# Kernel optimization log

Measured on AMD Instinct MI355X. Metric: run time of the kernel, lower is better.

## Reference

```python
import jax, jax.numpy as jnp
import numpy as np

N_NODES = 100000
N_FEATURES = 64
HIDDEN = 32
N_CLASSES = 10


def cheb_conv(x, row, col, W0, W1, b):
    """PyG ChebConv with K=2, sym normalization, lambda_max=2.0.

    L = I - D^-1/2 A D^-1/2 ; L_hat = 2L/lambda_max - I = -D^-1/2 A D^-1/2.
    out = x @ W0 + (L_hat x) @ W1 + b
    """
    N = x.shape[0]
    ew = jnp.where(row == col, 0.0, 1.0)  # remove_self_loops
    deg = jax.ops.segment_sum(ew, row, num_segments=N)
    dis = jnp.where(deg > 0, jax.lax.rsqrt(jnp.maximum(deg, 1.0)), 0.0)
    w = -(dis[row] * ew * dis[col])  # [E] scaled-Laplacian off-diagonal weights
    Tx1 = jax.ops.segment_sum(w[:, None] * x[row], col, num_segments=N)  # [N, F]
    return x @ W0 + Tx1 @ W1 + b


def _glorot(key, shape):
    fan_in, fan_out = shape
    s = jnp.sqrt(6.0 / (fan_in + fan_out))
    return jax.random.uniform(key, shape, jnp.float32, -s, s)


def setup_inputs() -> dict:
    key = jax.random.key(0)
    ks = jax.random.split(key, 8)
    x = jax.random.normal(ks[0], (N_NODES, N_FEATURES), dtype=jnp.float32)
    edge_index = jax.random.randint(ks[1], (2, 3200000), 0, N_NODES, dtype=jnp.int64)
    return {
        "x": x,
        "edge_index": edge_index,
        "W0_1": _glorot(ks[2], (N_FEATURES, HIDDEN)),
        "W1_1": _glorot(ks[3], (N_FEATURES, HIDDEN)),
        "b1": jnp.zeros((HIDDEN,), jnp.float32),
        "W0_2": _glorot(ks[4], (HIDDEN, N_CLASSES)),
        "W1_2": _glorot(ks[5], (HIDDEN, N_CLASSES)),
        "b2": jnp.zeros((N_CLASSES,), jnp.float32),
    }


def reference(x, edge_index, W0_1, W1_1, b1, W0_2, W1_2, b2):
    row, col = edge_index[0], edge_index[1]
    h = jax.nn.relu(cheb_conv(x, row, col, W0_1, W1_1, b1))
    x_latent = h
    # dropout is identity in eval mode
    out = cheb_conv(h, row, col, W0_2, W1_2, b2)
    return jax.nn.log_softmax(out, axis=1), x_latent
```

## Files before the change

kernel.cpp:

```cpp
#include <hip/hip_runtime.h>

#define NN   100000
#define FIN  64
#define HID  32
#define NCLS 10
#define BW   256
#define NB   391
#define HB   512

__global__ __launch_bounds__(256) void hist2_kernel(
        const int* __restrict__ row, const int* __restrict__ col,
        int* __restrict__ ghc, int* __restrict__ ghr, int E, int chunk) {
    __shared__ int lhc[NB], lhr[NB];
    for (int t = threadIdx.x; t < NB; t += 256) { lhc[t] = 0; lhr[t] = 0; }
    __syncthreads();
    int k = blockIdx.x;
    int base = k * chunk;
    int lim = base + chunk; if (lim > E) lim = E;
    for (int e = base + threadIdx.x; e < lim; e += 256) {
        int r = row[e], c = col[e];
        if (r != c) {
            atomicAdd(&lhc[c >> 8], 1);
            atomicAdd(&lhr[r >> 8], 1);
        }
    }
    __syncthreads();
    for (int t = threadIdx.x; t < NB; t += 256) {
        ghc[t * HB + k] = lhc[t];
        ghr[t * HB + k] = lhr[t];
    }
}

__global__ __launch_bounds__(512) void coffs_kernel(
        int* __restrict__ ghc, int* __restrict__ ghr,
        int* __restrict__ ctot, int* __restrict__ rtot) {
    __shared__ int sh[HB];
    int b = blockIdx.x, t = threadIdx.x;
    int v = ghc[b * HB + t];
    sh[t] = v;
    __syncthreads();
    for (int off = 1; off < HB; off <<= 1) {
        int u = (t >= off) ? sh[t - off] : 0;
        __syncthreads(); sh[t] += u; __syncthreads();
    }
    ghc[b * HB + t] = sh[t] - v;
    if (t == HB - 1) ctot[b] = sh[t];
    __syncthreads();
    int w = ghr[b * HB + t];
    sh[t] = w;
    __syncthreads();
    for (int off = 1; off < HB; off <<= 1) {
        int u = (t >= off) ? sh[t - off] : 0;
        __syncthreads(); sh[t] += u; __syncthreads();
    }
    ghr[b * HB + t] = sh[t] - w;
    if (t == HB - 1) rtot[b] = sh[t];
}

__global__ __launch_bounds__(512) void bscan_kernel(
        const int* __restrict__ ctot, const int* __restrict__ rtot,
        int* __restrict__ cbptr, int* __restrict__ rbptr,
        int* __restrict__ colptr) {
    __shared__ int sh[512];
    int t = threadIdx.x;
    int v = (t < NB) ? ctot[t] : 0;
    sh[t] = v;
    __syncthreads();
    for (int off = 1; off < 512; off <<= 1) {
        int u = (t >= off) ? sh[t - off] : 0;
        __syncthreads(); sh[t] += u; __syncthreads();
    }
    if (t < NB) cbptr[t] = sh[t] - v;
    if (t == NB - 1) { cbptr[NB] = sh[t]; colptr[NN] = sh[t]; }
    __syncthreads();
    int w = (t < NB) ? rtot[t] : 0;
    sh[t] = w;
    __syncthreads();
    for (int off = 1; off < 512; off <<= 1) {
        int u = (t >= off) ? sh[t - off] : 0;
        __syncthreads(); sh[t] += u; __syncthreads();
    }
    if (t < NB) rbptr[t] = sh[t] - w;
    if (t == NB - 1) rbptr[NB] = sh[t];
}

__global__ __launch_bounds__(256) void bucket2_kernel(
        const int* __restrict__ row, const int* __restrict__ col,
        const int* __restrict__ ghc, const int* __restrict__ ghr,
        const int* __restrict__ cbptr, const int* __restrict__ rbptr,
        int* __restrict__ pk, unsigned char* __restrict__ rkb,
        int E, int chunk) {
    __shared__ int lcc[NB], lcr[NB];
    int k = blockIdx.x;
    for (int t = threadIdx.x; t < NB; t += 256) {
        lcc[t] = cbptr[t] + ghc[t * HB + k];
        lcr[t] = rbptr[t] + ghr[t * HB + k];
    }
    __syncthreads();
    int base = k * chunk;
    int lim = base + chunk; if (lim > E) lim = E;
    for (int e = base + threadIdx.x; e < lim; e += 256) {
        int r = row[e], c = col[e];
        if (r != c) {
            int pc = atomicAdd(&lcc[c >> 8], 1);
            pk[pc] = (r << 8) | (c & 255);
            int pr = atomicAdd(&lcr[r >> 8], 1);
            rkb[pr] = (unsigned char)(r & 255);
        }
    }
}

__global__ __launch_bounds__(256) void countR_kernel(
        const unsigned char* __restrict__ rkb, const int* __restrict__ rbptr,
        float* __restrict__ dis) {
    __shared__ int cnt[BW];
    int b = blockIdx.x, t = threadIdx.x;
    cnt[t] = 0;
    __syncthreads();
    int s = rbptr[b], e = rbptr[b + 1];
    for (int i = s + t; i < e; i += 256) atomicAdd(&cnt[rkb[i]], 1);
    __syncthreads();
    int d = (b << 8) + t;
    if (d < NN) {
        int c = cnt[t];
        dis[d] = c > 0 ? rsqrtf((float)c) : 0.f;
    }
}

__global__ __launch_bounds__(256) void place2_kernel(
        const int* __restrict__ pk, const int* __restrict__ cbptr,
        int* __restrict__ colptr, int* __restrict__ srow) {
    __shared__ int lh[BW];
    __shared__ int incl[BW];
    __shared__ int lcur[BW];
    int b = blockIdx.x, t = threadIdx.x;
    int start = cbptr[b], end = cbptr[b + 1];
    lh[t] = 0;
    __syncthreads();
    for (int i = start + t; i < end; i += 256)
        atomicAdd(&lh[pk[i] & 255], 1);
    __syncthreads();
    int own = lh[t];
    incl[t] = own;
    __syncthreads();
    for (int off = 1; off < 256; off <<= 1) {
        int v = (t >= off) ? incl[t - off] : 0;
        __syncthreads(); incl[t] += v; __syncthreads();
    }
    int excl = start + incl[t] - own;
    int d = (b << 8) + t;
    if (d < NN) colptr[d] = excl;
    lcur[t] = excl;
    __syncthreads();
    for (int i = start + t; i < end; i += 256) {
        int p = pk[i];
        int pos = atomicAdd(&lcur[p & 255], 1);
        srow[pos] = p >> 8;
    }
}

__global__ __launch_bounds__(256) void mm1_kernel(
        const float* __restrict__ x, const float* __restrict__ dis,
        const float* __restrict__ W0, const float* __restrict__ W1,
        const float* __restrict__ b1, float* __restrict__ xw0,
        float* __restrict__ y1) {
    int n = blockIdx.x * 256 + threadIdx.x;
    if (n >= NN) return;
    float acc0[HID], acc1[HID];
#pragma unroll
    for (int j = 0; j < HID; ++j) { acc0[j] = b1[j]; acc1[j] = 0.f; }
    const float4* xr = (const float4*)(x + (size_t)n * FIN);
    for (int k4 = 0; k4 < FIN / 4; ++k4) {
        float4 xv = xr[k4];
        float xs[4] = {xv.x, xv.y, xv.z, xv.w};
#pragma unroll
        for (int kk = 0; kk < 4; ++kk) {
            const float* w0r = W0 + (k4 * 4 + kk) * HID;
            const float* w1r = W1 + (k4 * 4 + kk) * HID;
#pragma unroll
            for (int j = 0; j < HID; ++j) {
                acc0[j] += xs[kk] * w0r[j];
                acc1[j] += xs[kk] * w1r[j];
            }
        }
    }
    float dn = dis[n];
    float4* d0 = (float4*)(xw0 + (size_t)n * HID);
    float4* d1 = (float4*)(y1 + (size_t)n * HID);
#pragma unroll
    for (int j4 = 0; j4 < HID / 4; ++j4) {
        d0[j4] = make_float4(acc0[j4*4], acc0[j4*4+1], acc0[j4*4+2], acc0[j4*4+3]);
        d1[j4] = make_float4(dn*acc1[j4*4], dn*acc1[j4*4+1], dn*acc1[j4*4+2], dn*acc1[j4*4+3]);
    }
}

__global__ __launch_bounds__(256) void gatherH_kernel(
        const int* __restrict__ colptr, const int* __restrict__ srow,
        const float* __restrict__ dis, const float* __restrict__ y1,
        const float* __restrict__ xw0, float* __restrict__ h) {
    int lane = threadIdx.x & 63;
    int sub = lane >> 5, f = lane & 31;
    int c = __builtin_amdgcn_readfirstlane(blockIdx.x * 4 + (threadIdx.x >> 6));
    if (c >= NN) return;
    int start = colptr[c], end = colptr[c + 1];
    float a0 = 0.f, a1 = 0.f;
    int i = start + sub;
    for (; i + 2 < end; i += 4) {
        int r0 = srow[i], r1 = srow[i + 2];
        a0 += y1[(size_t)r0 * HID + f];
        a1 += y1[(size_t)r1 * HID + f];
    }
    for (; i < end; i += 2) a0 += y1[(size_t)srow[i] * HID + f];
    float tot = a0 + a1;
    tot += __shfl_xor(tot, 32);
    if (lane < 32) {
        float v = xw0[(size_t)c * HID + f] - dis[c] * tot;
        h[(size_t)c * HID + f] = fmaxf(v, 0.f);
    }
}

__global__ __launch_bounds__(256) void mm2_kernel(
        const float* __restrict__ h, const float* __restrict__ dis,
        const float* __restrict__ W0, const float* __restrict__ W1,
        const float* __restrict__ b2, float* __restrict__ hw0,
        float* __restrict__ y2) {
    int n = blockIdx.x * 256 + threadIdx.x;
    if (n >= NN) return;
    float acc0[NCLS], acc1[NCLS];
#pragma unroll
    for (int j = 0; j < NCLS; ++j) { acc0[j] = b2[j]; acc1[j] = 0.f; }
    const float4* hr = (const float4*)(h + (size_t)n * HID);
#pragma unroll
    for (int k4 = 0; k4 < HID / 4; ++k4) {
        float4 hv = hr[k4];
        float hs[4] = {hv.x, hv.y, hv.z, hv.w};
#pragma unroll
        for (int kk = 0; kk < 4; ++kk) {
            const float* w0r = W0 + (k4 * 4 + kk) * NCLS;
            const float* w1r = W1 + (k4 * 4 + kk) * NCLS;
#pragma unroll
            for (int j = 0; j < NCLS; ++j) {
                acc0[j] += hs[kk] * w0r[j];
                acc1[j] += hs[kk] * w1r[j];
            }
        }
    }
    float dn = dis[n];
    float* hd = hw0 + (size_t)n * NCLS;
#pragma unroll
    for (int j = 0; j < NCLS; ++j) hd[j] = acc0[j];
    float4* yd = (float4*)(y2 + (size_t)n * 16);
    float v[16];
#pragma unroll
    for (int j = 0; j < NCLS; ++j) v[j] = dn * acc1[j];
#pragma unroll
    for (int j = NCLS; j < 16; ++j) v[j] = 0.f;
#pragma unroll
    for (int j4 = 0; j4 < 4; ++j4)
        yd[j4] = make_float4(v[j4*4], v[j4*4+1], v[j4*4+2], v[j4*4+3]);
}

__global__ __launch_bounds__(256) void gatherOut_kernel(
        const int* __restrict__ colptr, const int* __restrict__ srow,
        const float* __restrict__ dis, const float* __restrict__ y2,
        const float* __restrict__ hw0, float* __restrict__ out) {
    int lane = threadIdx.x & 63;
    int sub = lane >> 4, f = lane & 15;
    int c = __builtin_amdgcn_readfirstlane(blockIdx.x * 4 + (threadIdx.x >> 6));
    if (c >= NN) return;
    int start = colptr[c], end = colptr[c + 1];
    float a0 = 0.f, a1 = 0.f;
    int i = start + sub;
    for (; i + 4 < end; i += 8) {
        int r0 = srow[i], r1 = srow[i + 4];
        a0 += y2[(size_t)r0 * 16 + f];
        a1 += y2[(size_t)r1 * 16 + f];
    }
    for (; i < end; i += 4) a0 += y2[(size_t)srow[i] * 16 + f];
    float tot = a0 + a1;
    tot += __shfl_xor(tot, 16);
    tot += __shfl_xor(tot, 32);
    float val = (f < NCLS ? hw0[(size_t)c * NCLS + f] : 0.f) - dis[c] * tot;
    float mv = (f < NCLS) ? val : -INFINITY;
    mv = fmaxf(mv, __shfl_xor(mv, 1));
    mv = fmaxf(mv, __shfl_xor(mv, 2));
    mv = fmaxf(mv, __shfl_xor(mv, 4));
    mv = fmaxf(mv, __shfl_xor(mv, 8));
    float ev = (f < NCLS) ? expf(val - mv) : 0.f;
    ev += __shfl_xor(ev, 1);
    ev += __shfl_xor(ev, 2);
    ev += __shfl_xor(ev, 4);
    ev += __shfl_xor(ev, 8);
    float lse = mv + logf(ev);
    if (lane < 16 && f < NCLS) out[(size_t)c * NCLS + f] = val - lse;
}

extern "C" void kernel_launch(void* const* d_in, const int* in_sizes, int n_in,
                              void* d_out, int out_size, void* d_ws, size_t ws_size,
                              hipStream_t stream) {
    const float* x    = (const float*)d_in[0];
    const int*   ei   = (const int*)d_in[1];
    const float* W0_1 = (const float*)d_in[2];
    const float* W1_1 = (const float*)d_in[3];
    const float* b1   = (const float*)d_in[4];
    const float* W0_2 = (const float*)d_in[5];
    const float* W1_2 = (const float*)d_in[6];
    const float* b2   = (const float*)d_in[7];

    const int E = in_sizes[1] / 2;
    const int* row = ei;
    const int* col = ei + E;

    int*   colptr = (int*)d_ws;
    float* dis    = (float*)(colptr + NN + 8);
    int*   cbptr  = (int*)(dis + NN);
    int*   rbptr  = cbptr + 512;
    int*   ctot   = rbptr + 512;
    int*   rtot   = ctot + 512;
    int*   srow   = rtot + 512;
    int*   C      = srow + E;
    int*   ghc    = C;
    int*   ghr    = ghc + NB * HB;
    int*   pk     = ghr + NB * HB;
    unsigned char* rkb = (unsigned char*)(pk + E);
    float* xw0    = (float*)C;
    float* y1     = xw0 + (size_t)NN * HID;
    float* hw0    = y1 + (size_t)NN * HID;
    float* y2     = hw0 + (size_t)NN * NCLS;

    float* out_ls = (float*)d_out;
    float* h      = out_ls + (size_t)NN * NCLS;

    int chunk = (E + HB - 1) / HB;

    hist2_kernel<<<HB, 256, 0, stream>>>(row, col, ghc, ghr, E, chunk);
    coffs_kernel<<<NB, 512, 0, stream>>>(ghc, ghr, ctot, rtot);
    bscan_kernel<<<1, 512, 0, stream>>>(ctot, rtot, cbptr, rbptr, colptr);
    bucket2_kernel<<<HB, 256, 0, stream>>>(row, col, ghc, ghr, cbptr, rbptr,
                                           pk, rkb, E, chunk);
    countR_kernel<<<NB, 256, 0, stream>>>(rkb, rbptr, dis);
    place2_kernel<<<NB, 256, 0, stream>>>(pk, cbptr, colptr, srow);

    mm1_kernel<<<(NN + 255) / 256, 256, 0, stream>>>(x, dis, W0_1, W1_1, b1, xw0, y1);
    gatherH_kernel<<<(NN + 3) / 4, 256, 0, stream>>>(colptr, srow, dis, y1, xw0, h);
    mm2_kernel<<<(NN + 255) / 256, 256, 0, stream>>>(h, dis, W0_2, W1_2, b2, hw0, y2);
    gatherOut_kernel<<<(NN + 3) / 4, 256, 0, stream>>>(colptr, srow, dis, y2, hw0, out_ls);
}
```

Baseline: 426.3 us.

## Drop CSR placement; aggregate from column buckets into LDS tiles with bf16 messages

Removes the place2 pass that built a full per-column CSR. Aggregation now reads the bucketed packed edges directly, with column buckets narrowed to 128 nodes, and accumulates into a shared-memory tile using LDS atomics before the fused epilogue. The intermediate per-node messages y1/y2 are stored as bf16 to halve gather traffic. This saves a full edge pass and gather bandwidth, at the cost of LDS atomic contention, more buckets in the histogram and scan stages, and reduced precision in the aggregated values.

```diff
diff --git a/kernel.cpp b/kernel.cpp
--- a/kernel.cpp
+++ b/kernel.cpp
@@ -1,18 +1,30 @@
 #include <hip/hip_runtime.h>
 
-#define NN   100000
-#define FIN  64
-#define HID  32
-#define NCLS 10
-#define BW   256
-#define NB   391
-#define HB   512
+#define NN    100000
+#define FIN   64
+#define HID   32
+#define NCLS  10
+#define CBW   128
+#define NBC   782
+#define RBW   256
+#define NBR   391
+#define HB    512
+
+__device__ __forceinline__ unsigned short f2bf(float x) {
+    unsigned u = __float_as_uint(x);
+    u = (u + 0x7FFFu + ((u >> 16) & 1u)) >> 16;
+    return (unsigned short)u;
+}
+__device__ __forceinline__ float bf2f(unsigned short s) {
+    return __uint_as_float(((unsigned)s) << 16);
+}
 
 __global__ __launch_bounds__(256) void hist2_kernel(
         const int* __restrict__ row, const int* __restrict__ col,
         int* __restrict__ ghc, int* __restrict__ ghr, int E, int chunk) {
-    __shared__ int lhc[NB], lhr[NB];
-    for (int t = threadIdx.x; t < NB; t += 256) { lhc[t] = 0; lhr[t] = 0; }
+    __shared__ int lhc[NBC], lhr[NBR];
+    for (int t = threadIdx.x; t < NBC; t += 256) lhc[t] = 0;
+    for (int t = threadIdx.x; t < NBR; t += 256) lhr[t] = 0;
     __syncthreads();
     int k = blockIdx.x;
     int base = k * chunk;
@@ -20,15 +32,13 @@
     for (int e = base + threadIdx.x; e < lim; e += 256) {
         int r = row[e], c = col[e];
         if (r != c) {
-            atomicAdd(&lhc[c >> 8], 1);
+            atomicAdd(&lhc[c >> 7], 1);
             atomicAdd(&lhr[r >> 8], 1);
         }
     }
     __syncthreads();
-    for (int t = threadIdx.x; t < NB; t += 256) {
-        ghc[t * HB + k] = lhc[t];
-        ghr[t * HB + k] = lhr[t];
-    }
+    for (int t = threadIdx.x; t < NBC; t += 256) ghc[t * HB + k] = lhc[t];
+    for (int t = threadIdx.x; t < NBR; t += 256) ghr[t * HB + k] = lhr[t];
 }
 
 __global__ __launch_bounds__(512) void coffs_kernel(
@@ -45,43 +55,44 @@
     }
     ghc[b * HB + t] = sh[t] - v;
     if (t == HB - 1) ctot[b] = sh[t];
-    __syncthreads();
-    int w = ghr[b * HB + t];
-    sh[t] = w;
-    __syncthreads();
-    for (int off = 1; off < HB; off <<= 1) {
+    if (b < NBR) {
+        __syncthreads();
+        int w = ghr[b * HB + t];
+        sh[t] = w;
+        __syncthreads();
+        for (int off = 1; off < HB; off <<= 1) {
+            int u = (t >= off) ? sh[t - off] : 0;
+            __syncthreads(); sh[t] += u; __syncthreads();
+        }
+        ghr[b * HB + t] = sh[t] - w;
+        if (t == HB - 1) rtot[b] = sh[t];
+    }
+}
+
+__global__ __launch_bounds__(1024) void bscan_kernel(
+        const int* __restrict__ ctot, const int* __restrict__ rtot,
+        int* __restrict__ cbptr, int* __restrict__ rbptr) {
+    __shared__ int sh[1024];
+    int t = threadIdx.x;
+    int v = (t < NBC) ? ctot[t] : 0;
+    sh[t] = v;
+    __syncthreads();
+    for (int off = 1; off < 1024; off <<= 1) {
         int u = (t >= off) ? sh[t - off] : 0;
         __syncthreads(); sh[t] += u; __syncthreads();
     }
-    ghr[b * HB + t] = sh[t] - w;
-    if (t == HB - 1) rtot[b] = sh[t];
-}
-
-__global__ __launch_bounds__(512) void bscan_kernel(
-        const int* __restrict__ ctot, const int* __restrict__ rtot,
-        int* __restrict__ cbptr, int* __restrict__ rbptr,
-        int* __restrict__ colptr) {
-    __shared__ int sh[512];
-    int t = threadIdx.x;
-    int v = (t < NB) ? ctot[t] : 0;
-    sh[t] = v;
-    __syncthreads();
-    for (int off = 1; off < 512; off <<= 1) {
+    if (t < NBC) cbptr[t] = sh[t] - v;
+    if (t == NBC - 1) cbptr[NBC] = sh[t];
+    __syncthreads();
+    int w = (t < NBR) ? rtot[t] : 0;
+    sh[t] = w;
+    __syncthreads();
+    for (int off = 1; off < 1024; off <<= 1) {
         int u = (t >= off) ? sh[t - off] : 0;
         __syncthreads(); sh[t] += u; __syncthreads();
     }
-    if (t < NB) cbptr[t] = sh[t] - v;
-    if (t == NB - 1) { cbptr[NB] = sh[t]; colptr[NN] = sh[t]; }
-    __syncthreads();
-    int w = (t < NB) ? rtot[t] : 0;
-    sh[t] = w;
-    __syncthreads();
-    for (int off = 1; off < 512; off <<= 1) {
-        int u = (t >= off) ? sh[t - off] : 0;
-        __syncthreads(); sh[t] += u; __syncthreads();
-    }
-    if (t < NB) rbptr[t] = sh[t] - w;
-    if (t == NB - 1) rbptr[NB] = sh[t];
+    if (t < NBR) rbptr[t] = sh[t] - w;
+    if (t == NBR - 1) rbptr[NBR] = sh[t];
 }
 
 __global__ __launch_bounds__(256) void bucket2_kernel(
@@ -90,20 +101,18 @@
         const int* __restrict__ cbptr, const int* __restrict__ rbptr,
         int* __restrict__ pk, unsigned char* __restrict__ rkb,
         int E, int chunk) {
-    __shared__ int lcc[NB], lcr[NB];
+    __shared__ int lcc[NBC], lcr[NBR];
     int k = blockIdx.x;
-    for (int t = threadIdx.x; t < NB; t += 256) {
-        lcc[t] = cbptr[t] + ghc[t * HB + k];
-        lcr[t] = rbptr[t] + ghr[t * HB + k];
-    }
+    for (int t = threadIdx.x; t < NBC; t += 256) lcc[t] = cbptr[t] + ghc[t * HB + k];
+    for (int t = threadIdx.x; t < NBR; t += 256) lcr[t] = rbptr[t] + ghr[t * HB + k];
     __syncthreads();
     int base = k * chunk;
     int lim = base + chunk; if (lim > E) lim = E;
     for (int e = base + threadIdx.x; e < lim; e += 256) {
         int r = row[e], c = col[e];
         if (r != c) {
-            int pc = atomicAdd(&lcc[c >> 8], 1);
-            pk[pc] = (r << 8) | (c & 255);
+            int pc = atomicAdd(&lcc[c >> 7], 1);
+            pk[pc] = (r << 7) | (c & 127);
             int pr = atomicAdd(&lcr[r >> 8], 1);
             rkb[pr] = (unsigned char)(r & 255);
         }
@@ -113,7 +122,7 @@
 __global__ __launch_bounds__(256) void countR_kernel(
         const unsigned char* __restrict__ rkb, const int* __restrict__ rbptr,
         float* __restrict__ dis) {
-    __shared__ int cnt[BW];
+    __shared__ int cnt[RBW];
     int b = blockIdx.x, t = threadIdx.x;
     cnt[t] = 0;
     __syncthreads();
@@ -127,43 +136,11 @@
     }
 }
 
-__global__ __launch_bounds__(256) void place2_kernel(
-        const int* __restrict__ pk, const int* __restrict__ cbptr,
-        int* __restrict__ colptr, int* __restrict__ srow) {
-    __shared__ int lh[BW];
-    __shared__ int incl[BW];
-    __shared__ int lcur[BW];
-    int b = blockIdx.x, t = threadIdx.x;
-    int start = cbptr[b], end = cbptr[b + 1];
-    lh[t] = 0;
-    __syncthreads();
-    for (int i = start + t; i < end; i += 256)
-        atomicAdd(&lh[pk[i] & 255], 1);
-    __syncthreads();
-    int own = lh[t];
-    incl[t] = own;
-    __syncthreads();
-    for (int off = 1; off < 256; off <<= 1) {
-        int v = (t >= off) ? incl[t - off] : 0;
-        __syncthreads(); incl[t] += v; __syncthreads();
-    }
-    int excl = start + incl[t] - own;
-    int d = (b << 8) + t;
-    if (d < NN) colptr[d] = excl;
-    lcur[t] = excl;
-    __syncthreads();
-    for (int i = start + t; i < end; i += 256) {
-        int p = pk[i];
-        int pos = atomicAdd(&lcur[p & 255], 1);
-        srow[pos] = p >> 8;
-    }
-}
-
 __global__ __launch_bounds__(256) void mm1_kernel(
         const float* __restrict__ x, const float* __restrict__ dis,
         const float* __restrict__ W0, const float* __restrict__ W1,
         const float* __restrict__ b1, float* __restrict__ xw0,
-        float* __restrict__ y1) {
+        unsigned* __restrict__ y1b) {
     int n = blockIdx.x * 256 + threadIdx.x;
     if (n >= NN) return;
     float acc0[HID], acc1[HID];
@@ -186,36 +163,66 @@
     }
     float dn = dis[n];
     float4* d0 = (float4*)(xw0 + (size_t)n * HID);
-    float4* d1 = (float4*)(y1 + (size_t)n * HID);
-#pragma unroll
-    for (int j4 = 0; j4 < HID / 4; ++j4) {
+#pragma unroll
+    for (int j4 = 0; j4 < HID / 4; ++j4)
         d0[j4] = make_float4(acc0[j4*4], acc0[j4*4+1], acc0[j4*4+2], acc0[j4*4+3]);
-        d1[j4] = make_float4(dn*acc1[j4*4], dn*acc1[j4*4+1], dn*acc1[j4*4+2], dn*acc1[j4*4+3]);
-    }
-}
-
-__global__ __launch_bounds__(256) void gatherH_kernel(
-        const int* __restrict__ colptr, const int* __restrict__ srow,
-        const float* __restrict__ dis, const float* __restrict__ y1,
-        const float* __restrict__ xw0, float* __restrict__ h) {
-    int lane = threadIdx.x & 63;
-    int sub = lane >> 5, f = lane & 31;
-    int c = __builtin_amdgcn_readfirstlane(blockIdx.x * 4 + (threadIdx.x >> 6));
-    if (c >= NN) return;
-    int start = colptr[c], end = colptr[c + 1];
-    float a0 = 0.f, a1 = 0.f;
-    int i = start + sub;
-    for (; i + 2 < end; i += 4) {
-        int r0 = srow[i], r1 = srow[i + 2];
-        a0 += y1[(size_t)r0 * HID + f];
-        a1 += y1[(size_t)r1 * HID + f];
-    }
-    for (; i < end; i += 2) a0 += y1[(size_t)srow[i] * HID + f];
-    float tot = a0 + a1;
-    tot += __shfl_xor(tot, 32);
-    if (lane < 32) {
-        float v = xw0[(size_t)c * HID + f] - dis[c] * tot;
-        h[(size_t)c * HID + f] = fmaxf(v, 0.f);
+    unsigned pw[16];
+#pragma unroll
+    for (int j2 = 0; j2 < 16; ++j2)
+        pw[j2] = (unsigned)f2bf(dn * acc1[2*j2]) | ((unsigned)f2bf(dn * acc1[2*j2+1]) << 16);
+    uint4* yd = (uint4*)(y1b + (size_t)n * 16);
+#pragma unroll
+    for (int q = 0; q < 4; ++q)
+        yd[q] = make_uint4(pw[q*4], pw[q*4+1], pw[q*4+2], pw[q*4+3]);
+}
+
+__global__ __launch_bounds__(256) void fgH_kernel(
+        const int* __restrict__ pk, const int* __restrict__ cbptr,
+        const unsigned short* __restrict__ y1b, const float* __restrict__ xw0,
+        const float* __restrict__ dis, float* __restrict__ h) {
+    __shared__ float tile[CBW * 33];
+    int tid = threadIdx.x;
+    for (int q = tid; q < CBW * 33; q += 256) tile[q] = 0.f;
+    int b = blockIdx.x;
+    int start = cbptr[b], end = cbptr[b + 1];
+    int slot = tid >> 5;
+    int f = tid & 31;
+    __syncthreads();
+    int i = start + slot;
+    for (; i + 24 < end; i += 32) {
+        int p0 = pk[i], p1 = pk[i + 8], p2 = pk[i + 16], p3 = pk[i + 24];
+        float v0 = bf2f(y1b[(size_t)(p0 >> 7) * HID + f]);
+        float v1 = bf2f(y1b[(size_t)(p1 >> 7) * HID + f]);
+        float v2 = bf2f(y1b[(size_t)(p2 >> 7) * HID + f]);
+        float v3 = bf2f(y1b[(size_t)(p3 >> 7) * HID + f]);
+        atomicAdd(&tile[(p0 & 127) * 33 + f], v0);
+        atomicAdd(&tile[(p1 & 127) * 33 + f], v1);
+        atomicAdd(&tile[(p2 & 127) * 33 + f], v2);
+        atomicAdd(&tile[(p3 & 127) * 33 + f], v3);
+    }
+    for (; i < end; i += 8) {
+        int p = pk[i];
+        atomicAdd(&tile[(p & 127) * 33 + f], bf2f(y1b[(size_t)(p >> 7) * HID + f]));
+    }
+    __syncthreads();
+    int d = tid >> 1;
+    int g = b * CBW + d;
+    if (g < NN) {
+        int hf = (tid & 1) * 16;
+        float dc = dis[g];
+        const float4* xs = (const float4*)(xw0 + (size_t)g * HID + hf);
+        float4* hd = (float4*)(h + (size_t)g * HID + hf);
+        const float* tr = &tile[d * 33 + hf];
+#pragma unroll
+        for (int q4 = 0; q4 < 4; ++q4) {
+            float4 xv = xs[q4];
+            float4 o;
+            o.x = fmaxf(xv.x - dc * tr[q4*4 + 0], 0.f);
+            o.y = fmaxf(xv.y - dc * tr[q4*4 + 1], 0.f);
+            o.z = fmaxf(xv.z - dc * tr[q4*4 + 2], 0.f);
+            o.w = fmaxf(xv.w - dc * tr[q4*4 + 3], 0.f);
+            hd[q4] = o;
+        }
     }
 }
 
@@ -223,7 +230,7 @@
         const float* __restrict__ h, const float* __restrict__ dis,
         const float* __restrict__ W0, const float* __restrict__ W1,
         const float* __restrict__ b2, float* __restrict__ hw0,
-        float* __restrict__ y2) {
+        unsigned* __restrict__ y2b) {
     int n = blockIdx.x * 256 + threadIdx.x;
     if (n >= NN) return;
     float acc0[NCLS], acc1[NCLS];
@@ -249,50 +256,68 @@
     float* hd = hw0 + (size_t)n * NCLS;
 #pragma unroll
     for (int j = 0; j < NCLS; ++j) hd[j] = acc0[j];
-    float4* yd = (float4*)(y2 + (size_t)n * 16);
     float v[16];
 #pragma unroll
     for (int j = 0; j < NCLS; ++j) v[j] = dn * acc1[j];
 #pragma unroll
     for (int j = NCLS; j < 16; ++j) v[j] = 0.f;
-#pragma unroll
-    for (int j4 = 0; j4 < 4; ++j4)
-        yd[j4] = make_float4(v[j4*4], v[j4*4+1], v[j4*4+2], v[j4*4+3]);
-}
-
-__global__ __launch_bounds__(256) void gatherOut_kernel(
-        const int* __restrict__ colptr, const int* __restrict__ srow,
-        const float* __restrict__ dis, const float* __restrict__ y2,
-        const float* __restrict__ hw0, float* __restrict__ out) {
-    int lane = threadIdx.x & 63;
-    int sub = lane >> 4, f = lane & 15;
-    int c = __builtin_amdgcn_readfirstlane(blockIdx.x * 4 + (threadIdx.x >> 6));
-    if (c >= NN) return;
-    int start = colptr[c], end = colptr[c + 1];
-    float a0 = 0.f, a1 = 0.f;
-    int i = start + sub;
-    for (; i + 4 < end; i += 8) {
-        int r0 = srow[i], r1 = srow[i + 4];
-        a0 += y2[(size_t)r0 * 16 + f];
-        a1 += y2[(size_t)r1 * 16 + f];
-    }
-    for (; i < end; i += 4) a0 += y2[(size_t)srow[i] * 16 + f];
-    float tot = a0 + a1;
-    tot += __shfl_xor(tot, 16);
-    tot += __shfl_xor(tot, 32);
-    float val = (f < NCLS ? hw0[(size_t)c * NCLS + f] : 0.f) - dis[c] * tot;
-    float mv = (f < NCLS) ? val : -INFINITY;
-    mv = fmaxf(mv, __shfl_xor(mv, 1));
-    mv = fmaxf(mv, __shfl_xor(mv, 2));
-    mv = fmaxf(mv, __shfl_xor(mv, 4));
-    mv = fmaxf(mv, __shfl_xor(mv, 8));
-    float ev = (f < NCLS) ? expf(val - mv) : 0.f;
-    ev += __shfl_xor(ev, 1);
-    ev += __shfl_xor(ev, 2);
-    ev += __shfl_xor(ev, 4);
-    ev += __shfl_xor(ev, 8);
-    float lse = mv + logf(ev);
-    if (lane < 16 && f < NCLS) out[(size_t)c * NCLS + f] = val - lse;
+    unsigned pw[8];
+#pragma unroll
+    for (int j2 = 0; j2 < 8; ++j2)
+        pw[j2] = (unsigned)f2bf(v[2*j2]) | ((unsigned)f2bf(v[2*j2+1]) << 16);
+    uint4* yd = (uint4*)(y2b + (size_t)n * 8);
+    yd[0] = make_uint4(pw[0], pw[1], pw[2], pw[3]);
+    yd[1] = make_uint4(pw[4], pw[5], pw[6], pw[7]);
+}
+
+__global__ __launch_bounds__(256) void fgO_kernel(
+        const int* __restrict__ pk, const int* __restrict__ cbptr,
+        const unsigned short* __restrict__ y2b, const float* __restrict__ hw0,
+        const float* __restrict__ dis, float* __restrict__ out) {
+    __shared__ float tile[CBW * 17];
+    int tid = threadIdx.x;
+    for (int q = tid; q < CBW * 17; q += 256) tile[q] = 0.f;
+    int b = blockIdx.x;
+    int start = cbptr[b], end = cbptr[b + 1];
+    int slot = tid >> 4;
+    int f = tid & 15;
+    __syncthreads();
+    int i = start + slot;
+    for (; i + 16 < end; i += 32) {
+        int p0 = pk[i], p1 = pk[i + 16];
+        float v0 = bf2f(y2b[(size_t)(p0 >> 7) * 16 + f]);
+        float v1 = bf2f(y2b[(size_t)(p1 >> 7) * 16 + f]);
+        atomicAdd(&tile[(p0 & 127) * 17 + f], v0);
+        atomicAdd(&tile[(p1 & 127) * 17 + f], v1);
+    }
+    for (; i < end; i += 16) {
+        int p = pk[i];
+        atomicAdd(&tile[(p & 127) * 17 + f], bf2f(y2b[(size_t)(p >> 7) * 16 + f]));
+    }
+    __syncthreads();
+    int nmax = NN - b * CBW; if (nmax > CBW) nmax = CBW;
+    if (tid < nmax) {
+        int g = b * CBW + tid;
+        float dc = dis[g];
+        const float* hs = hw0 + (size_t)g * NCLS;
+        float val[NCLS];
+#pragma unroll
+        for (int j = 0; j < NCLS; ++j) val[j] = hs[j] - dc * tile[tid * 17 + j];
+        float m = val[0];
+#pragma unroll
+        for (int j = 1; j < NCLS; ++j) m = fmaxf(m, val[j]);
+        float s = 0.f;
+#pragma unroll
+        for (int j = 0; j < NCLS; ++j) s += expf(val[j] - m);
+        float lse = m + logf(s);
+#pragma unroll
+        for (int j = 0; j < NCLS; ++j) tile[tid * 17 + j] = val[j] - lse;
+    }
+    __syncthreads();
+    int total = nmax * NCLS;
+    float* ob = out + (size_t)b * CBW * NCLS;
+    for (int q = tid; q < total; q += 256)
+        ob[q] = tile[(q / NCLS) * 17 + q % NCLS];
 }
 
 extern "C" void kernel_launch(void* const* d_in, const int* in_sizes, int n_in,
@@ -311,22 +336,19 @@
     const int* row = ei;
     const int* col = ei + E;
 
-    int*   colptr = (int*)d_ws;
-    float* dis    = (float*)(colptr + NN + 8);
-    int*   cbptr  = (int*)(dis + NN);
-    int*   rbptr  = cbptr + 512;
-    int*   ctot   = rbptr + 512;
-    int*   rtot   = ctot + 512;
-    int*   srow   = rtot + 512;
-    int*   C      = srow + E;
-    int*   ghc    = C;
-    int*   ghr    = ghc + NB * HB;
-    int*   pk     = ghr + NB * HB;
+    float* dis   = (float*)d_ws;
+    int* cbptr   = (int*)d_ws + 100016;
+    int* rbptr   = cbptr + 800;
+    int* ctot    = rbptr + 400;
+    int* rtot    = ctot + 800;
+    int* ghc     = rtot + 400;
+    int* ghr     = ghc + NBC * HB;
+    int* pk      = ghr + NBR * HB;
     unsigned char* rkb = (unsigned char*)(pk + E);
-    float* xw0    = (float*)C;
-    float* y1     = xw0 + (size_t)NN * HID;
-    float* hw0    = y1 + (size_t)NN * HID;
-    float* y2     = hw0 + (size_t)NN * NCLS;
+    float* xw0   = (float*)(pk + E + E / 4);
+    unsigned* y1b = (unsigned*)(xw0 + (size_t)NN * HID);
+    float* hw0   = (float*)(y1b + (size_t)NN * 16);
+    unsigned* y2b = (unsigned*)(hw0 + (size_t)NN * NCLS);
 
     float* out_ls = (float*)d_out;
     float* h      = out_ls + (size_t)NN * NCLS;
@@ -334,15 +356,16 @@
     int chunk = (E + HB - 1) / HB;
 
     hist2_kernel<<<HB, 256, 0, stream>>>(row, col, ghc, ghr, E, chunk);
-    coffs_kernel<<<NB, 512, 0, stream>>>(ghc, ghr, ctot, rtot);
-    bscan_kernel<<<1, 512, 0, stream>>>(ctot, rtot, cbptr, rbptr, colptr);
+    coffs_kernel<<<NBC, 512, 0, stream>>>(ghc, ghr, ctot, rtot);
+    bscan_kernel<<<1, 1024, 0, stream>>>(ctot, rtot, cbptr, rbptr);
     bucket2_kernel<<<HB, 256, 0, stream>>>(row, col, ghc, ghr, cbptr, rbptr,
                                            pk, rkb, E, chunk);
-    countR_kernel<<<NB, 256, 0, stream>>>(rkb, rbptr, dis);
-    place2_kernel<<<NB, 256, 0, stream>>>(pk, cbptr, colptr, srow);
-
-    mm1_kernel<<<(NN + 255) / 256, 256, 0, stream>>>(x, dis, W0_1, W1_1, b1, xw0, y1);
-    gatherH_kernel<<<(NN + 3) / 4, 256, 0, stream>>>(colptr, srow, dis, y1, xw0, h);
-    mm2_kernel<<<(NN + 255) / 256, 256, 0, stream>>>(h, dis, W0_2, W1_2, b2, hw0, y2);
-    gatherOut_kernel<<<(NN + 3) / 4, 256, 0, stream>>>(colptr, srow, dis, y2, hw0, out_ls);
-}
+    countR_kernel<<<NBR, 256, 0, stream>>>(rkb, rbptr, dis);
+
+    mm1_kernel<<<(NN + 255) / 256, 256, 0, stream>>>(x, dis, W0_1, W1_1, b1, xw0, y1b);
+    fgH_kernel<<<NBC, 256, 0, stream>>>(pk, cbptr, (const unsigned short*)y1b,
+                                        xw0, dis, h);
+    mm2_kernel<<<(NN + 255) / 256, 256, 0, stream>>>(h, dis, W0_2, W1_2, b2, hw0, y2b);
+    fgO_kernel<<<NBC, 256, 0, stream>>>(pk, cbptr, (const unsigned short*)y2b,
+                                        hw0, dis, out_ls);
+}
```

Result: slower. 1.252 ms (+193.6%).

## Store gathered neighbor features in bf16 to halve gather traffic

Applied to the files above, without the earlier changes.

The dis-scaled message tensors y1 and y2 are now packed as bf16 pairs in mm1/mm2, and both gather kernels read packed words, accumulating two features per lane in fp32. This halves the bytes fetched per edge in the two random-access aggregation passes, which dominate over 3.2M edges. The colptr[NN] sentinel write also moves from bscan to place2. The cost is bf16 rounding of neighbor messages, which may loosen accuracy against the fp32 reference.

```diff
diff --git a/kernel.cpp b/kernel.cpp
--- a/kernel.cpp
+++ b/kernel.cpp
@@ -7,6 +7,18 @@
 #define BW   256
 #define NB   391
 #define HB   512
+
+__device__ __forceinline__ unsigned short f2bf(float x) {
+    unsigned u = __float_as_uint(x);
+    u = (u + 0x7FFFu + ((u >> 16) & 1u)) >> 16;
+    return (unsigned short)u;
+}
+__device__ __forceinline__ float bfLo(unsigned u) {
+    return __uint_as_float(u << 16);
+}
+__device__ __forceinline__ float bfHi(unsigned u) {
+    return __uint_as_float(u & 0xFFFF0000u);
+}
 
 __global__ __launch_bounds__(256) void hist2_kernel(
         const int* __restrict__ row, const int* __restrict__ col,
@@ -59,8 +71,7 @@
 
 __global__ __launch_bounds__(512) void bscan_kernel(
         const int* __restrict__ ctot, const int* __restrict__ rtot,
-        int* __restrict__ cbptr, int* __restrict__ rbptr,
-        int* __restrict__ colptr) {
+        int* __restrict__ cbptr, int* __restrict__ rbptr) {
     __shared__ int sh[512];
     int t = threadIdx.x;
     int v = (t < NB) ? ctot[t] : 0;
@@ -71,7 +82,7 @@
         __syncthreads(); sh[t] += u; __syncthreads();
     }
     if (t < NB) cbptr[t] = sh[t] - v;
-    if (t == NB - 1) { cbptr[NB] = sh[t]; colptr[NN] = sh[t]; }
+    if (t == NB - 1) cbptr[NB] = sh[t];
     __syncthreads();
     int w = (t < NB) ? rtot[t] : 0;
     sh[t] = w;
@@ -157,13 +168,14 @@
         int pos = atomicAdd(&lcur[p & 255], 1);
         srow[pos] = p >> 8;
     }
+    if (b == 0 && t == 0) colptr[NN] = cbptr[NB];
 }
 
 __global__ __launch_bounds__(256) void mm1_kernel(
         const float* __restrict__ x, const float* __restrict__ dis,
         const float* __restrict__ W0, const float* __restrict__ W1,
         const float* __restrict__ b1, float* __restrict__ xw0,
-        float* __restrict__ y1) {
+        unsigned* __restrict__ y1b) {
     int n = blockIdx.x * 256 + threadIdx.x;
     if (n >= NN) return;
     float acc0[HID], acc1[HID];
@@ -186,36 +198,52 @@
     }
     float dn = dis[n];
     float4* d0 = (float4*)(xw0 + (size_t)n * HID);
-    float4* d1 = (float4*)(y1 + (size_t)n * HID);
-#pragma unroll
-    for (int j4 = 0; j4 < HID / 4; ++j4) {
+#pragma unroll
+    for (int j4 = 0; j4 < HID / 4; ++j4)
         d0[j4] = make_float4(acc0[j4*4], acc0[j4*4+1], acc0[j4*4+2], acc0[j4*4+3]);
-        d1[j4] = make_float4(dn*acc1[j4*4], dn*acc1[j4*4+1], dn*acc1[j4*4+2], dn*acc1[j4*4+3]);
-    }
+    unsigned pw[16];
+#pragma unroll
+    for (int j2 = 0; j2 < 16; ++j2)
+        pw[j2] = (unsigned)f2bf(dn * acc1[2*j2]) | ((unsigned)f2bf(dn * acc1[2*j2+1]) << 16);
+    uint4* yd = (uint4*)(y1b + (size_t)n * 16);
+#pragma unroll
+    for (int q = 0; q < 4; ++q)
+        yd[q] = make_uint4(pw[q*4], pw[q*4+1], pw[q*4+2], pw[q*4+3]);
 }
 
 __global__ __launch_bounds__(256) void gatherH_kernel(
         const int* __restrict__ colptr, const int* __restrict__ srow,
-        const float* __restrict__ dis, const float* __restrict__ y1,
+        const float* __restrict__ dis, const unsigned* __restrict__ y1b,
         const float* __restrict__ xw0, float* __restrict__ h) {
     int lane = threadIdx.x & 63;
-    int sub = lane >> 5, f = lane & 31;
+    int sub = lane >> 4;
+    int f2 = lane & 15;
     int c = __builtin_amdgcn_readfirstlane(blockIdx.x * 4 + (threadIdx.x >> 6));
     if (c >= NN) return;
     int start = colptr[c], end = colptr[c + 1];
-    float a0 = 0.f, a1 = 0.f;
+    float a0 = 0.f, a1 = 0.f, b0 = 0.f, b1 = 0.f;
     int i = start + sub;
-    for (; i + 2 < end; i += 4) {
-        int r0 = srow[i], r1 = srow[i + 2];
-        a0 += y1[(size_t)r0 * HID + f];
-        a1 += y1[(size_t)r1 * HID + f];
-    }
-    for (; i < end; i += 2) a0 += y1[(size_t)srow[i] * HID + f];
-    float tot = a0 + a1;
-    tot += __shfl_xor(tot, 32);
-    if (lane < 32) {
-        float v = xw0[(size_t)c * HID + f] - dis[c] * tot;
-        h[(size_t)c * HID + f] = fmaxf(v, 0.f);
+    for (; i + 4 < end; i += 8) {
+        unsigned u0 = y1b[(size_t)srow[i] * 16 + f2];
+        unsigned u1 = y1b[(size_t)srow[i + 4] * 16 + f2];
+        a0 += bfLo(u0); a1 += bfHi(u0);
+        b0 += bfLo(u1); b1 += bfHi(u1);
+    }
+    for (; i < end; i += 4) {
+        unsigned u = y1b[(size_t)srow[i] * 16 + f2];
+        a0 += bfLo(u); a1 += bfHi(u);
+    }
+    a0 += b0; a1 += b1;
+    a0 += __shfl_xor(a0, 16); a1 += __shfl_xor(a1, 16);
+    a0 += __shfl_xor(a0, 32); a1 += __shfl_xor(a1, 32);
+    if (lane < 16) {
+        float dc = dis[c];
+        const float2* xs = (const float2*)(xw0 + (size_t)c * HID + 2 * f2);
+        float2 xv = xs[0];
+        float2 o;
+        o.x = fmaxf(xv.x - dc * a0, 0.f);
+        o.y = fmaxf(xv.y - dc * a1, 0.f);
+        *(float2*)(h + (size_t)c * HID + 2 * f2) = o;
     }
 }
 
@@ -223,7 +251,7 @@
         const float* __restrict__ h, const float* __restrict__ dis,
         const float* __restrict__ W0, const float* __restrict__ W1,
         const float* __restrict__ b2, float* __restrict__ hw0,
-        float* __restrict__ y2) {
+        unsigned* __restrict__ y2b) {
     int n = blockIdx.x * 256 + threadIdx.x;
     if (n >= NN) return;
     float acc0[NCLS], acc1[NCLS];
@@ -249,50 +277,63 @@
     float* hd = hw0 + (size_t)n * NCLS;
 #pragma unroll
     for (int j = 0; j < NCLS; ++j) hd[j] = acc0[j];
-    float4* yd = (float4*)(y2 + (size_t)n * 16);
     float v[16];
 #pragma unroll
     for (int j = 0; j < NCLS; ++j) v[j] = dn * acc1[j];
 #pragma unroll
     for (int j = NCLS; j < 16; ++j) v[j] = 0.f;
-#pragma unroll
-    for (int j4 = 0; j4 < 4; ++j4)
-        yd[j4] = make_float4(v[j4*4], v[j4*4+1], v[j4*4+2], v[j4*4+3]);
+    unsigned pw[8];
+#pragma unroll
+    for (int j2 = 0; j2 < 8; ++j2)
+        pw[j2] = (unsigned)f2bf(v[2*j2]) | ((unsigned)f2bf(v[2*j2+1]) << 16);
+    uint4* yd = (uint4*)(y2b + (size_t)n * 8);
+    yd[0] = make_uint4(pw[0], pw[1], pw[2], pw[3]);
+    yd[1] = make_uint4(pw[4], pw[5], pw[6], pw[7]);
 }
 
 __global__ __launch_bounds__(256) void gatherOut_kernel(
         const int* __restrict__ colptr, const int* __restrict__ srow,
-        const float* __restrict__ dis, const float* __restrict__ y2,
+        const float* __restrict__ dis, const unsigned* __restrict__ y2b,
         const float* __restrict__ hw0, float* __restrict__ out) {
     int lane = threadIdx.x & 63;
-    int sub = lane >> 4, f = lane & 15;
+    int sub = lane >> 3;
+    int f2 = lane & 7;
     int c = __builtin_amdgcn_readfirstlane(blockIdx.x * 4 + (threadIdx.x >> 6));
     if (c >= NN) return;
     int start = colptr[c], end = colptr[c + 1];
-    float a0 = 0.f, a1 = 0.f;
+    float a0 = 0.f, a1 = 0.f, b0 = 0.f, b1 = 0.f;
     int i = start + sub;
-    for (; i + 4 < end; i += 8) {
-        int r0 = srow[i], r1 = srow[i + 4];
-        a0 += y2[(size_t)r0 * 16 + f];
-        a1 += y2[(size_t)r1 * 16 + f];
-    }
-    for (; i < end; i += 4) a0 += y2[(size_t)srow[i] * 16 + f];
-    float tot = a0 + a1;
-    tot += __shfl_xor(tot, 16);
-    tot += __shfl_xor(tot, 32);
-    float val = (f < NCLS ? hw0[(size_t)c * NCLS + f] : 0.f) - dis[c] * tot;
-    float mv = (f < NCLS) ? val : -INFINITY;
-    mv = fmaxf(mv, __shfl_xor(mv, 1));
-    mv = fmaxf(mv, __shfl_xor(mv, 2));
-    mv = fmaxf(mv, __shfl_xor(mv, 4));
-    mv = fmaxf(mv, __shfl_xor(mv, 8));
-    float ev = (f < NCLS) ? expf(val - mv) : 0.f;
-    ev += __shfl_xor(ev, 1);
-    ev += __shfl_xor(ev, 2);
-    ev += __shfl_xor(ev, 4);
-    ev += __shfl_xor(ev, 8);
-    float lse = mv + logf(ev);
-    if (lane < 16 && f < NCLS) out[(size_t)c * NCLS + f] = val - lse;
+    for (; i + 8 < end; i += 16) {
+        unsigned u0 = y2b[(size_t)srow[i] * 8 + f2];
+        unsigned u1 = y2b[(size_t)srow[i + 8] * 8 + f2];
+        a0 += bfLo(u0); a1 += bfHi(u0);
+        b0 += bfLo(u1); b1 += bfHi(u1);
+    }
+    for (; i < end; i += 8) {
+        unsigned u = y2b[(size_t)srow[i] * 8 + f2];
+        a0 += bfLo(u); a1 += bfHi(u);
+    }
+    a0 += b0; a1 += b1;
+    a0 += __shfl_xor(a0, 8);  a1 += __shfl_xor(a1, 8);
+    a0 += __shfl_xor(a0, 16); a1 += __shfl_xor(a1, 16);
+    a0 += __shfl_xor(a0, 32); a1 += __shfl_xor(a1, 32);
+    float dc = dis[c];
+    int j0 = 2 * f2, j1 = 2 * f2 + 1;
+    float v0 = (j0 < NCLS) ? hw0[(size_t)c * NCLS + j0] - dc * a0 : -INFINITY;
+    float v1 = (j1 < NCLS) ? hw0[(size_t)c * NCLS + j1] - dc * a1 : -INFINITY;
+    float m = fmaxf(v0, v1);
+    m = fmaxf(m, __shfl_xor(m, 1));
+    m = fmaxf(m, __shfl_xor(m, 2));
+    m = fmaxf(m, __shfl_xor(m, 4));
+    float s = ((j0 < NCLS) ? expf(v0 - m) : 0.f) + ((j1 < NCLS) ? expf(v1 - m) : 0.f);
+    s += __shfl_xor(s, 1);
+    s += __shfl_xor(s, 2);
+    s += __shfl_xor(s, 4);
+    float lse = m + logf(s);
+    if (lane < 8) {
+        if (j0 < NCLS) out[(size_t)c * NCLS + j0] = v0 - lse;
+        if (j1 < NCLS) out[(size_t)c * NCLS + j1] = v1 - lse;
+    }
 }
 
 extern "C" void kernel_launch(void* const* d_in, const int* in_sizes, int n_in,
@@ -324,9 +365,9 @@
     int*   pk     = ghr + NB * HB;
     unsigned char* rkb = (unsigned char*)(pk + E);
     float* xw0    = (float*)C;
-    float* y1     = xw0 + (size_t)NN * HID;
-    float* hw0    = y1 + (size_t)NN * HID;
-    float* y2     = hw0 + (size_t)NN * NCLS;
+    unsigned* y1b = (unsigned*)(xw0 + (size_t)NN * HID);
+    float* hw0    = (float*)(y1b + (size_t)NN * 16);
+    unsigned* y2b = (unsigned*)(hw0 + (size_t)NN * NCLS);
 
     float* out_ls = (float*)d_out;
     float* h      = out_ls + (size_t)NN * NCLS;
@@ -335,14 +376,14 @@
 
     hist2_kernel<<<HB, 256, 0, stream>>>(row, col, ghc, ghr, E, chunk);
     coffs_kernel<<<NB, 512, 0, stream>>>(ghc, ghr, ctot, rtot);
-    bscan_kernel<<<1, 512, 0, stream>>>(ctot, rtot, cbptr, rbptr, colptr);
+    bscan_kernel<<<1, 512, 0, stream>>>(ctot, rtot, cbptr, rbptr);
     bucket2_kernel<<<HB, 256, 0, stream>>>(row, col, ghc, ghr, cbptr, rbptr,
                                            pk, rkb, E, chunk);
     countR_kernel<<<NB, 256, 0, stream>>>(rkb, rbptr, dis);
     place2_kernel<<<NB, 256, 0, stream>>>(pk, cbptr, colptr, srow);
 
-    mm1_kernel<<<(NN + 255) / 256, 256, 0, stream>>>(x, dis, W0_1, W1_1, b1, xw0, y1);
-    gatherH_kernel<<<(NN + 3) / 4, 256, 0, stream>>>(colptr, srow, dis, y1, xw0, h);
-    mm2_kernel<<<(NN + 255) / 256, 256, 0, stream>>>(h, dis, W0_2, W1_2, b2, hw0, y2);
-    gatherOut_kernel<<<(NN + 3) / 4, 256, 0, stream>>>(colptr, srow, dis, y2, hw0, out_ls);
-}
+    mm1_kernel<<<(NN + 255) / 256, 256, 0, stream>>>(x, dis, W0_1, W1_1, b1, xw0, y1b);
+    gatherH_kernel<<<(NN + 3) / 4, 256, 0, stream>>>(colptr, srow, dis, y1b, xw0, h);
+    mm2_kernel<<<(NN + 255) / 256, 256, 0, stream>>>(h, dis, W0_2, W1_2, b2, hw0, y2b);
+    gatherOut_kernel<<<(NN + 3) / 4, 256, 0, stream>>>(colptr, srow, dis, y2b, hw0, out_ls);
+}
```

Result: faster. 375.9 us (-11.8%).
